# Kernel tuning notes

Hardware: AMD Instinct MI355X
Metric: run time of the kernel (lower is better)

## Reference

```python
import jax, jax.numpy as jnp
from jax import lax
import numpy as np

N, E = 10000, 120000
IN_DIM = 128
HID = 32        # hidden_dim
HEADS = 8
OUT = 32        # out_dim
HD = HID * HEADS  # 256
EPS = 1e-5


def _bn(x, g, b):
    # BatchNorm1d (training-mode batch stats, deterministic reference)
    mu = x.mean(0)
    var = x.var(0)
    return g * (x - mu) * lax.rsqrt(var + EPS) + b


def _seg_softmax(logits, seg, n):
    # softmax over edges grouped by destination node, per head
    m = jax.ops.segment_max(logits, seg, num_segments=n)
    ex = jnp.exp(logits - m[seg])
    s = jax.ops.segment_sum(ex, seg, num_segments=n)
    return ex / (s[seg] + 1e-16)


def _gat_layer(h, src, dst, fc_w, a_l, a_r, bn_g, bn_b, heads, out, residual):
    n = h.shape[0]
    h_in = h
    feat = (h @ fc_w).reshape(n, heads, out)      # [N,H,D]
    el = (feat * a_l).sum(-1)                     # [N,H]
    er = (feat * a_r).sum(-1)
    logits = jax.nn.leaky_relu(el[src] + er[dst], 0.2)  # [E,H]
    alpha = _seg_softmax(logits, dst, n)
    rst = jax.ops.segment_sum(alpha[..., None] * feat[src], dst, num_segments=n)
    rst = rst.reshape(n, heads * out)
    rst = _bn(rst, bn_g, bn_b)
    rst = jax.nn.elu(rst)
    if residual:
        rst = h_in + rst
    return rst


def setup_inputs():
    key = jax.random.key(0)
    ks = jax.random.split(key, 20)
    s = 0.02
    d = {}
    d["h"] = jax.random.normal(ks[0], (N, IN_DIM), jnp.float32)
    d["e"] = jax.random.normal(ks[1], (E, IN_DIM), jnp.float32)
    d["src"] = jax.random.randint(ks[2], (E,), 0, N, jnp.int32)
    d["dst"] = jax.random.randint(ks[3], (E,), 0, N, jnp.int32)
    d["W_emb"] = jax.random.normal(ks[4], (IN_DIM, HD)) * s
    d["b_emb"] = jnp.zeros((HD,))
    d["W_p1"] = jax.random.normal(ks[5], (IN_DIM, HID * HID)) * s
    d["b_p1"] = jnp.zeros((HID * HID,))
    d["W_p2"] = jax.random.normal(ks[6], (IN_DIM, HID)) * s
    d["b_p2"] = jnp.zeros((HID,))
    d["W_conv"] = jax.random.normal(ks[7], (1, 2, 3)) * s  # Conv1d(2->1,k=3)
    d["b_conv"] = jnp.zeros((1,))
    d["W_ep2"] = jax.random.normal(ks[8], (IN_DIM, HD)) * s
    d["b_ep2"] = jnp.zeros((HD,))
    d["W_ep3"] = jax.random.normal(ks[9], (HID, HD)) * s
    d["b_ep3"] = jnp.zeros((HD,))
    d["bn_g"] = jnp.ones((HD,))
    d["bn_b"] = jnp.zeros((HD,))
    d["fc1"] = jax.random.normal(ks[10], (HD, HD)) * s
    d["al1"] = jax.random.normal(ks[11], (HEADS, HID)) * s
    d["ar1"] = jax.random.normal(ks[12], (HEADS, HID)) * s
    d["g1"] = jnp.ones((HD,))
    d["b1"] = jnp.zeros((HD,))
    d["fc2"] = jax.random.normal(ks[13], (HD, OUT)) * s
    d["al2"] = jax.random.normal(ks[14], (1, OUT)) * s
    d["ar2"] = jax.random.normal(ks[15], (1, OUT)) * s
    d["g2"] = jnp.ones((OUT,))
    d["b2"] = jnp.zeros((OUT,))
    return d


def reference(h, e, src, dst, W_emb, b_emb, W_p1, b_p1, W_p2, b_p2,
              W_conv, b_conv, W_ep2, b_ep2, W_ep3, b_ep3, bn_g, bn_b,
              fc1, al1, ar1, g1, b1, fc2, al2, ar2, g2, b2):
    # local edge feature: Conv1d over stacked (src,dst) node feats
    edge = jnp.stack([h[src], h[dst]], axis=1)  # [E,2,IN_DIM]
    conv = lax.conv_general_dilated(edge, W_conv, (1,), [(1, 1)],
                                    dimension_numbers=("NCH", "OIH", "NCH"))
    lr_local = conv[:, 0, :] + b_conv[0]         # [E,IN_DIM]
    lr_e_local = lr_local @ W_ep2 + b_ep2        # [E,HD]
    # low-rank global affinity: mm[i,j,k] = sum_d p1[i,k,d]*p2[j,d],
    # gathered only at edges (same math as the dense NxNxHID tensor)
    p1 = (h @ W_p1 + b_p1).reshape(-1, HID, HID)  # [N,HID,HID]
    p2 = h @ W_p2 + b_p2                          # [N,HID]
    lr_glob = jnp.einsum("ekd,ed->ek", p1[src], p2[dst])  # [E,HID]
    lr_e_global = lr_glob @ W_ep3 + b_ep3        # [E,HD]
    e_feat = jax.nn.relu(_bn(lr_e_local + lr_e_global, bn_g, bn_b))
    del e_feat  # default 'dgl' GATLayer ignores e; kept for faithfulness of math
    hh = h @ W_emb + b_emb                       # embedding_h
    hh = _gat_layer(hh, src, dst, fc1, al1, ar1, g1, b1, HEADS, HID, True)
    hh = _gat_layer(hh, src, dst, fc2, al2, ar2, g2, b2, 1, OUT, False)
    return hh
```

## Files before the change

kernel.cpp:

```cpp
#include <hip/hip_runtime.h>
#include <hip/hip_bf16.h>
#include <math.h>


#define HDIM 256
#define NHEADS 8
#define ODIM 32

typedef unsigned short u16;
typedef __attribute__((ext_vector_type(8))) short short8;
typedef __attribute__((ext_vector_type(4))) float f32x4;

__device__ __forceinline__ float bf2f(u16 u) { return __uint_as_float(((unsigned)u) << 16); }
__device__ __forceinline__ u16 f2bf(float f) {
    unsigned x = __float_as_uint(f);
    return (u16)((x + 0x7FFFu + ((x >> 16) & 1u)) >> 16);
}

__global__ __launch_bounds__(256) void prep_kernel(const float* __restrict__ in_h, const float* __restrict__ W_emb,
                                                   const float* __restrict__ fc1, const float* __restrict__ fc2,
                                                   const int* __restrict__ dstv, int* __restrict__ deg,
                                                   u16* __restrict__ Ah, u16* __restrict__ Bemb,
                                                   u16* __restrict__ Bfc1, u16* __restrict__ Bfc2,
                                                   int n4, int E, int N) {
    int job = blockIdx.y;
    int idx = blockIdx.x * 256 + threadIdx.x;
    if (job == 0) {
        if (idx >= n4) return;
        float4 v = ((const float4*)in_h)[idx];
        ushort4 o = {f2bf(v.x), f2bf(v.y), f2bf(v.z), f2bf(v.w)};
        ((ushort4*)Ah)[idx] = o;
        return;
    }
    if (job == 4) {
        if (idx < E) {
            unsigned d = (unsigned)dstv[idx];
            if (d < (unsigned)N) atomicAdd(&deg[d], 1);
        }
        return;
    }
    const float* B;
    u16* O;
    int K, NC;
    if (job == 1) { B = W_emb; O = Bemb; K = 128; NC = 256; }
    else if (job == 2) { B = fc1; O = Bfc1; K = 256; NC = 256; }
    else { B = fc2; O = Bfc2; K = 256; NC = 32; }
    int KB = K / 32;
    int TOT = (NC / 16) * KB * 64;
    if (idx >= TOT) return;
    int lane = idx & 63;
    int kb = (idx >> 6) % KB;
    int ct = (idx >> 6) / KB;
    int n = ct * 16 + (lane & 15);
    int k0 = kb * 32 + (lane >> 4) * 8;
    u16* dst = O + (size_t)idx * 8;
#pragma unroll
    for (int j = 0; j < 8; j++) dst[j] = f2bf(B[(size_t)(k0 + j) * NC + n]);
}

__global__ __launch_bounds__(256) void scan_kernel(const int* __restrict__ deg, int* __restrict__ offs,
                                                   int* __restrict__ cursor, int n) {
    __shared__ int wsum[4];
    int t = threadIdx.x;
    int chunk = (n + 255) / 256;
    int lo = t * chunk, hi = lo + chunk;
    if (hi > n) hi = n;
    if (lo > n) lo = n;
    int s = 0;
    for (int i = lo; i < hi; i++) s += deg[i];
    int v = s;
#pragma unroll
    for (int d = 1; d < 64; d <<= 1) {
        int nb = __shfl_up(v, d, 64);
        if ((t & 63) >= d) v += nb;
    }
    if ((t & 63) == 63) wsum[t >> 6] = v;
    __syncthreads();
    int woff = 0;
#pragma unroll
    for (int w = 0; w < 4; w++)
        if (w < (t >> 6)) woff += wsum[w];
    int run = woff + v - s;
    for (int i = lo; i < hi; i++) {
        offs[i] = run;
        cursor[i] = run;
        run += deg[i];
    }
    if (t == 255) offs[n] = run;
}

__global__ __launch_bounds__(256) void fused_emb_fc1(const u16* __restrict__ Ah, const u16* __restrict__ Bemb,
                                                     const float* __restrict__ bemb, const u16* __restrict__ Bfc1,
                                                     const float* __restrict__ al, const float* __restrict__ ar,
                                                     u16* __restrict__ hh, u16* __restrict__ feat1,
                                                     u16* __restrict__ el, u16* __restrict__ er,
                                                     const int* __restrict__ src, const int* __restrict__ dstv,
                                                     int* __restrict__ cursor, int* __restrict__ srcs,
                                                     int M, int NB, int E, int N) {
    if ((int)blockIdx.x >= NB) {
        int i = ((int)blockIdx.x - NB) * 256 + (int)threadIdx.x;
        if (i < E) {
            unsigned d = (unsigned)dstv[i];
            if (d < (unsigned)N) {
                int p = atomicAdd(&cursor[d], 1);
                if ((unsigned)p < (unsigned)E) srcs[p] = src[i];
            }
        }
        return;
    }
    __shared__ u16 tile[16 * 256];
    const int t = threadIdx.x;
    const int lane = t & 63, w = t >> 6;
    const int rb = (int)blockIdx.x * 16;
    const int m = lane & 15, q = lane >> 4;
    const int arow = rb + m;

    short8 a0[4];
#pragma unroll
    for (int kb = 0; kb < 4; kb++) {
        if (arow < M) a0[kb] = *(const short8*)(Ah + (size_t)arow * 128 + kb * 32 + q * 8);
        else a0[kb] = (short8){0, 0, 0, 0, 0, 0, 0, 0};
    }
    const short8* B8 = (const short8*)Bemb;
#pragma unroll
    for (int ct2 = 0; ct2 < 4; ct2++) {
        const int ct = w * 4 + ct2;
        f32x4 acc = {0.f, 0.f, 0.f, 0.f};
#pragma unroll
        for (int kb = 0; kb < 4; kb++)
            acc = __builtin_amdgcn_mfma_f32_16x16x32_bf16(a0[kb], B8[(ct * 4 + kb) * 64 + lane], acc, 0, 0, 0);
        float bv = bemb[ct * 16 + m];
#pragma unroll
        for (int r = 0; r < 4; r++) {
            int rl = q * 4 + r;
            int ro = rb + rl;
            u16 hv = 0;
            if (ro < M) {
                hv = f2bf(acc[r] + bv);
                hh[(size_t)ro * 256 + ct * 16 + m] = hv;
            }
            int byte = rl * 512 + (ct * 16 + m) * 2;
            tile[(byte ^ ((rl & 7) << 4)) >> 1] = hv;
        }
    }
    __syncthreads();

    short8 af[8];
    {
        int rl = m;
#pragma unroll
        for (int kb = 0; kb < 8; kb++) {
            int byte = rl * 512 + kb * 64 + q * 16;
            af[kb] = *(const short8*)(tile + ((byte ^ ((rl & 7) << 4)) >> 1));
        }
    }
    __syncthreads();

    const short8* Bf = (const short8*)Bfc1;
#pragma unroll
    for (int ct2 = 0; ct2 < 4; ct2++) {
        const int ct = w * 4 + ct2;
        f32x4 acc = {0.f, 0.f, 0.f, 0.f};
#pragma unroll
        for (int kb = 0; kb < 8; kb++)
            acc = __builtin_amdgcn_mfma_f32_16x16x32_bf16(af[kb], Bf[(ct * 8 + kb) * 64 + lane], acc, 0, 0, 0);
#pragma unroll
        for (int r = 0; r < 4; r++) {
            int rl = q * 4 + r;
            int ro = rb + rl;
            u16 v = 0;
            if (ro < M) {
                v = f2bf(acc[r]);
                feat1[(size_t)ro * 256 + ct * 16 + m] = v;
            }
            tile[rl * 256 + ct * 16 + m] = v;
        }
    }
    __syncthreads();

    if (t < 128) {
        int nl = t >> 3, h2 = t & 7;
        int node = rb + nl;
        if (node < M) {
            float a_ = 0.f, b_ = 0.f;
#pragma unroll
            for (int d = 0; d < 32; d++) {
                float fv = bf2f(tile[nl * 256 + h2 * 32 + d]);
                a_ += fv * al[h2 * 32 + d];
                b_ += fv * ar[h2 * 32 + d];
            }
            el[node * 8 + h2] = f2bf(a_);
            er[node * 8 + h2] = f2bf(b_);
        }
    }
}

__device__ __forceinline__ float edgew(float l) {
    l = (l > 0.f) ? l : 0.2f * l;
    l = fminf(fmaxf(l, -30.f), 30.f);
    return __expf(l);
}

__global__ __launch_bounds__(256) void agg1_fused(const u16* __restrict__ feat, const u16* __restrict__ el,
                                                  const u16* __restrict__ er, const int* __restrict__ offs,
                                                  const int* __restrict__ srcs, u16* __restrict__ rst, int N, int E) {
    const int node = blockIdx.x * 4 + (threadIdx.x >> 6);
    const int lane = threadIdx.x & 63;
    if (node >= N) return;
    const int h = lane >> 3;
    int beg = offs[node], end = offs[node + 1];
    if (beg < 0) beg = 0;
    if (end > E) end = E;
    float ern = bf2f(er[node * 8 + h]);
    float ax = 0.f, ay = 0.f, az = 0.f, aw = 0.f, sw = 0.f;
    int j = beg;
    int end4 = beg + ((end - beg) & ~3);
    for (; j < end4; j += 4) {
        int s0 = srcs[j], s1 = srcs[j + 1], s2 = srcs[j + 2], s3 = srcs[j + 3];
        unsigned c0 = (unsigned)s0 < (unsigned)N, c1 = (unsigned)s1 < (unsigned)N;
        unsigned c2 = (unsigned)s2 < (unsigned)N, c3 = (unsigned)s3 < (unsigned)N;
        s0 = c0 ? s0 : 0; s1 = c1 ? s1 : 0; s2 = c2 ? s2 : 0; s3 = c3 ? s3 : 0;
        u16 e0 = el[s0 * 8 + h], e1 = el[s1 * 8 + h], e2 = el[s2 * 8 + h], e3 = el[s3 * 8 + h];
        ushort4 f0 = *(const ushort4*)(feat + (size_t)s0 * 256 + lane * 4);
        ushort4 f1 = *(const ushort4*)(feat + (size_t)s1 * 256 + lane * 4);
        ushort4 f2 = *(const ushort4*)(feat + (size_t)s2 * 256 + lane * 4);
        ushort4 f3 = *(const ushort4*)(feat + (size_t)s3 * 256 + lane * 4);
        float w0 = c0 ? edgew(bf2f(e0) + ern) : 0.f;
        float w1 = c1 ? edgew(bf2f(e1) + ern) : 0.f;
        float w2 = c2 ? edgew(bf2f(e2) + ern) : 0.f;
        float w3 = c3 ? edgew(bf2f(e3) + ern) : 0.f;
        sw += w0 + w1 + w2 + w3;
        ax += w0 * bf2f(f0.x) + w1 * bf2f(f1.x) + w2 * bf2f(f2.x) + w3 * bf2f(f3.x);
        ay += w0 * bf2f(f0.y) + w1 * bf2f(f1.y) + w2 * bf2f(f2.y) + w3 * bf2f(f3.y);
        az += w0 * bf2f(f0.z) + w1 * bf2f(f1.z) + w2 * bf2f(f2.z) + w3 * bf2f(f3.z);
        aw += w0 * bf2f(f0.w) + w1 * bf2f(f1.w) + w2 * bf2f(f2.w) + w3 * bf2f(f3.w);
    }
    for (; j < end; j++) {
        int s = srcs[j];
        if ((unsigned)s >= (unsigned)N) continue;
        float wv = edgew(bf2f(el[s * 8 + h]) + ern);
        ushort4 f4 = *(const ushort4*)(feat + (size_t)s * 256 + lane * 4);
        sw += wv;
        ax += wv * bf2f(f4.x);
        ay += wv * bf2f(f4.y);
        az += wv * bf2f(f4.z);
        aw += wv * bf2f(f4.w);
    }
    float inv = 1.f / (sw + 1e-16f);
    ushort4 o;
    o.x = f2bf(ax * inv); o.y = f2bf(ay * inv); o.z = f2bf(az * inv); o.w = f2bf(aw * inv);
    *(ushort4*)(rst + (size_t)node * 256 + lane * 4) = o;
}

__global__ __launch_bounds__(256) void bn_stats256(const u16* __restrict__ X, float* __restrict__ stats,
                                                   int rows, int RPB) {
    int t = threadIdx.x;
    int rbeg = blockIdx.x * RPB;
    int rend = rbeg + RPB;
    if (rend > rows) rend = rows;
    float s = 0.f, s2 = 0.f;
    for (int r = rbeg; r < rend; r++) {
        float x = bf2f(X[(long)r * 256 + t]);
        s += x;
        s2 += x * x;
    }
    atomicAdd(&stats[t], s);
    atomicAdd(&stats[256 + t], s2);
}

__global__ __launch_bounds__(256) void bn_stats32(const float* __restrict__ X, float* __restrict__ stats,
                                                  int rows, int RPB) {
    __shared__ float ss[256], ss2[256];
    int t = threadIdx.x, c = t & 31, rs = t >> 5;
    int rbeg = blockIdx.x * RPB;
    int rend = rbeg + RPB;
    if (rend > rows) rend = rows;
    float s = 0.f, s2 = 0.f;
    for (int r = rbeg + rs; r < rend; r += 8) {
        float x = X[(long)r * 32 + c];
        s += x;
        s2 += x * x;
    }
    ss[t] = s;
    ss2[t] = s2;
    __syncthreads();
    if (t < 32) {
        for (int j = 32; j < 256; j += 32) { s += ss[t + j]; s2 += ss2[t + j]; }
        atomicAdd(&stats[c], s);
        atomicAdd(&stats[32 + c], s2);
    }
}

__global__ __launch_bounds__(256) void gemm_fc2_fused(const u16* __restrict__ rst, const u16* __restrict__ hh,
                                                      const float* __restrict__ stats, const float* __restrict__ g,
                                                      const float* __restrict__ b, const u16* __restrict__ Bsw,
                                                      const float* __restrict__ al2, const float* __restrict__ ar2,
                                                      float* __restrict__ feat2, float* __restrict__ el2,
                                                      float* __restrict__ er2, int M, float invN) {
    __shared__ float sc[256], sh[256];
    __shared__ float red[2][256];
    __shared__ float tile[16][32];
    const int t = threadIdx.x;
    {
        float mu = stats[t] * invN;
        float var = fmaxf(stats[256 + t] * invN - mu * mu, 0.f);
        float s = g[t] * rsqrtf(var + 1e-5f);
        sc[t] = s;
        sh[t] = b[t] - mu * s;
    }
    __syncthreads();
    const int lane = t & 63, w = t >> 6;
    const int ct = w & 1, kh = w >> 1;
    const int rb = (int)blockIdx.x * 16;
    const int m = lane & 15, q = lane >> 4;
    const int row = rb + m;
    short8 a[4];
#pragma unroll
    for (int j = 0; j < 4; j++) {
        if (row < M) {
            int k0 = (kh * 4 + j) * 32 + q * 8;
            ushort4 r01 = *(const ushort4*)(rst + (size_t)row * 256 + k0);
            ushort4 r23 = *(const ushort4*)(rst + (size_t)row * 256 + k0 + 4);
            ushort4 h01 = *(const ushort4*)(hh + (size_t)row * 256 + k0);
            ushort4 h23 = *(const ushort4*)(hh + (size_t)row * 256 + k0 + 4);
            u16 rv[8] = {r01.x, r01.y, r01.z, r01.w, r23.x, r23.y, r23.z, r23.w};
            u16 hv[8] = {h01.x, h01.y, h01.z, h01.w, h23.x, h23.y, h23.z, h23.w};
            short8 av;
#pragma unroll
            for (int jj = 0; jj < 8; jj++) {
                int c = k0 + jj;
                float y = sc[c] * bf2f(rv[jj]) + sh[c];
                y = (y > 0.f) ? y : expm1f(y);
                av[jj] = (short)f2bf(bf2f(hv[jj]) + y);
            }
            a[j] = av;
        } else a[j] = (short8){0, 0, 0, 0, 0, 0, 0, 0};
    }
    const short8* B8 = (const short8*)Bsw;
    f32x4 acc = {0.f, 0.f, 0.f, 0.f};
#pragma unroll
    for (int j = 0; j < 4; j++)
        acc = __builtin_amdgcn_mfma_f32_16x16x32_bf16(a[j], B8[(ct * 8 + kh * 4 + j) * 64 + lane], acc, 0, 0, 0);
    if (kh == 1) *(f32x4*)&red[ct][lane * 4] = acc;
    __syncthreads();
    if (kh == 0) {
        f32x4 p = *(const f32x4*)&red[ct][lane * 4];
#pragma unroll
        for (int r = 0; r < 4; r++) {
            int rl = q * 4 + r;
            int ro = rb + rl;
            float v = 0.f;
            if (ro < M) {
                v = acc[r] + p[r];
                feat2[(size_t)ro * 32 + ct * 16 + m] = v;
            }
            tile[rl][ct * 16 + m] = v;
        }
    }
    __syncthreads();
    if (t < 16) {
        int node = rb + t;
        if (node < M) {
            float a_ = 0.f, b_ = 0.f;
#pragma unroll
            for (int d = 0; d < 32; d++) {
                float fv = tile[t][d];
                a_ += fv * al2[d];
                b_ += fv * ar2[d];
            }
            el2[node] = a_;
            er2[node] = b_;
        }
    }
}

__global__ __launch_bounds__(256) void agg2_fused(const float* __restrict__ feat, const float* __restrict__ el,
                                                  const float* __restrict__ er, const int* __restrict__ offs,
                                                  const int* __restrict__ srcs, float* __restrict__ rst,
                                                  int N, int E) {
    const int t = threadIdx.x;
    const int node = blockIdx.x * 8 + (t >> 5);
    const int d = t & 31;
    if (node >= N) return;
    int beg = offs[node], end = offs[node + 1];
    if (beg < 0) beg = 0;
    if (end > E) end = E;
    float ern = er[node];
    float acc = 0.f, sw = 0.f;
#pragma unroll 2
    for (int j = beg; j < end; j++) {
        int s = srcs[j];
        if ((unsigned)s >= (unsigned)N) continue;
        float wv = edgew(el[s] + ern);
        sw += wv;
        acc += wv * feat[(size_t)s * 32 + d];
    }
    rst[(size_t)node * 32 + d] = acc / (sw + 1e-16f);
}

__global__ __launch_bounds__(256) void bn_apply2(const float* __restrict__ rst, const float* __restrict__ stats,
                                                 const float* __restrict__ g, const float* __restrict__ b,
                                                 float* __restrict__ out, int total, float invN) {
    int idx = blockIdx.x * 256 + threadIdx.x;
    if (idx >= total) return;
    int c = idx & 31;
    float mu = stats[c] * invN;
    float var = fmaxf(stats[32 + c] * invN - mu * mu, 0.f);
    float y = g[c] * (rst[idx] - mu) * rsqrtf(var + 1e-5f) + b[c];
    y = (y > 0.f) ? y : expm1f(y);
    out[idx] = y;
}

extern "C" void kernel_launch(void* const* d_in, const int* in_sizes, int n_in, void* d_out, int out_size, void* d_ws,
                              size_t ws_size, hipStream_t stream) {
    const int N = out_size / ODIM;
    const int E = in_sizes[2];

    const int* src = (const int*)d_in[2];
    const int* dst = (const int*)d_in[3];
    const float* in_h = (const float*)d_in[0];
    const float* W_emb = (const float*)d_in[4];  const float* b_emb = (const float*)d_in[5];
    const float* fc1 = (const float*)d_in[18];   const float* al1 = (const float*)d_in[19];
    const float* ar1 = (const float*)d_in[20];
    const float* g1 = (const float*)d_in[21];    const float* b1 = (const float*)d_in[22];
    const float* fc2 = (const float*)d_in[23];   const float* al2 = (const float*)d_in[24];
    const float* ar2 = (const float*)d_in[25];
    const float* g2 = (const float*)d_in[26];    const float* b2 = (const float*)d_in[27];
    float* out = (float*)d_out;

    char* base = (char*)d_ws;
    size_t off = 0;
    auto alloc = [&](size_t bytes) { void* p = base + off; off += (bytes + 63) & ~63ull; return p; };
    char* zb   = (char*)alloc((size_t)N * 4 + 512 * 4 + 64 * 4);
    int* deg   = (int*)zb;
    float* stats  = (float*)(zb + (size_t)N * 4);
    float* stats2 = stats + 512;
    int* offs  = (int*)alloc((size_t)(N + 1) * 4);
    int* cursor = (int*)alloc((size_t)N * 4);
    int* srcs  = (int*)alloc((size_t)E * 4);
    u16* Ah    = (u16*)alloc((size_t)N * 128 * 2);
    u16* Bemb  = (u16*)alloc((size_t)128 * 256 * 2);
    u16* Bfc1  = (u16*)alloc((size_t)256 * 256 * 2);
    u16* Bfc2  = (u16*)alloc((size_t)256 * 32 * 2);
    u16* hh    = (u16*)alloc((size_t)N * HDIM * 2);
    u16* feat1 = (u16*)alloc((size_t)N * HDIM * 2);
    u16* el1   = (u16*)alloc((size_t)N * 8 * 2);
    u16* er1   = (u16*)alloc((size_t)N * 8 * 2);
    u16* rst   = (u16*)alloc((size_t)N * HDIM * 2);
    float* feat2 = (float*)alloc((size_t)N * 32 * 4);
    float* el2 = (float*)alloc((size_t)N * 4);
    float* er2 = (float*)alloc((size_t)N * 4);
    float* rst2 = (float*)alloc((size_t)N * 32 * 4);

    const int NB16 = (N + 15) / 16;
    const int NBF = (E + 255) / 256;

    hipMemsetAsync(zb, 0, (size_t)N * 4 + 512 * 4 + 64 * 4, stream);
    prep_kernel<<<dim3((N * 128 / 4 + 255) / 256, 5), 256, 0, stream>>>(in_h, W_emb, fc1, fc2, dst, deg,
                                                                        Ah, Bemb, Bfc1, Bfc2, N * 128 / 4, E, N);
    scan_kernel<<<1, 256, 0, stream>>>(deg, offs, cursor, N);
    fused_emb_fc1<<<NB16 + NBF, 256, 0, stream>>>(Ah, Bemb, b_emb, Bfc1, al1, ar1, hh, feat1, el1, er1,
                                                  src, dst, cursor, srcs, N, NB16, E, N);
    agg1_fused<<<(N + 3) / 4, 256, 0, stream>>>(feat1, el1, er1, offs, srcs, rst, N, E);
    bn_stats256<<<(N + 39) / 40, 256, 0, stream>>>(rst, stats, N, 40);
    gemm_fc2_fused<<<NB16, 256, 0, stream>>>(rst, hh, stats, g1, b1, Bfc2, al2, ar2, feat2, el2, er2, N, 1.f / N);
    agg2_fused<<<(N + 7) / 8, 256, 0, stream>>>(feat2, el2, er2, offs, srcs, rst2, N, E);
    bn_stats32<<<(N + 63) / 64, 256, 0, stream>>>(rst2, stats2, N, 64);
    bn_apply2<<<(N * ODIM + 255) / 256, 256, 0, stream>>>(rst2, stats2, g2, b2, out, N * ODIM, 1.f / N);
}
```

Before: 252.0 us.

## Fuse all pipeline stages into one persistent kernel with grid barriers

Replaces the sequence of nine kernel launches with a single persistent megakernel. It is sized from occupancy queries and separates stages with a software grid-wide barrier built on an atomic counter and generation flag. Each former kernel becomes a grid-stride loop inside that one kernel. The goal is to remove launch overhead and inter-kernel gaps. The cost is a spin-wait barrier with a timeout guard, lower occupancy from the shared register budget, and a deadlock risk if the blocks are not all co-resident.

Measured after the change: 449.9 us. 1.79x slower.

```diff
diff --git a/kernel.cpp b/kernel.cpp
--- a/kernel.cpp
+++ b/kernel.cpp
@@ -4,7 +4,6 @@
 
 
 #define HDIM 256
-#define NHEADS 8
 #define ODIM 32
 
 typedef unsigned short u16;
@@ -16,399 +15,439 @@
     unsigned x = __float_as_uint(f);
     return (u16)((x + 0x7FFFu + ((x >> 16) & 1u)) >> 16);
 }
-
-__global__ __launch_bounds__(256) void prep_kernel(const float* __restrict__ in_h, const float* __restrict__ W_emb,
-                                                   const float* __restrict__ fc1, const float* __restrict__ fc2,
-                                                   const int* __restrict__ dstv, int* __restrict__ deg,
-                                                   u16* __restrict__ Ah, u16* __restrict__ Bemb,
-                                                   u16* __restrict__ Bfc1, u16* __restrict__ Bfc2,
-                                                   int n4, int E, int N) {
-    int job = blockIdx.y;
-    int idx = blockIdx.x * 256 + threadIdx.x;
-    if (job == 0) {
-        if (idx >= n4) return;
-        float4 v = ((const float4*)in_h)[idx];
-        ushort4 o = {f2bf(v.x), f2bf(v.y), f2bf(v.z), f2bf(v.w)};
-        ((ushort4*)Ah)[idx] = o;
-        return;
-    }
-    if (job == 4) {
-        if (idx < E) {
-            unsigned d = (unsigned)dstv[idx];
-            if (d < (unsigned)N) atomicAdd(&deg[d], 1);
-        }
-        return;
-    }
-    const float* B;
-    u16* O;
-    int K, NC;
-    if (job == 1) { B = W_emb; O = Bemb; K = 128; NC = 256; }
-    else if (job == 2) { B = fc1; O = Bfc1; K = 256; NC = 256; }
-    else { B = fc2; O = Bfc2; K = 256; NC = 32; }
-    int KB = K / 32;
-    int TOT = (NC / 16) * KB * 64;
-    if (idx >= TOT) return;
-    int lane = idx & 63;
-    int kb = (idx >> 6) % KB;
-    int ct = (idx >> 6) / KB;
-    int n = ct * 16 + (lane & 15);
-    int k0 = kb * 32 + (lane >> 4) * 8;
-    u16* dst = O + (size_t)idx * 8;
-#pragma unroll
-    for (int j = 0; j < 8; j++) dst[j] = f2bf(B[(size_t)(k0 + j) * NC + n]);
-}
-
-__global__ __launch_bounds__(256) void scan_kernel(const int* __restrict__ deg, int* __restrict__ offs,
-                                                   int* __restrict__ cursor, int n) {
-    __shared__ int wsum[4];
-    int t = threadIdx.x;
-    int chunk = (n + 255) / 256;
-    int lo = t * chunk, hi = lo + chunk;
-    if (hi > n) hi = n;
-    if (lo > n) lo = n;
-    int s = 0;
-    for (int i = lo; i < hi; i++) s += deg[i];
-    int v = s;
-#pragma unroll
-    for (int d = 1; d < 64; d <<= 1) {
-        int nb = __shfl_up(v, d, 64);
-        if ((t & 63) >= d) v += nb;
-    }
-    if ((t & 63) == 63) wsum[t >> 6] = v;
-    __syncthreads();
-    int woff = 0;
-#pragma unroll
-    for (int w = 0; w < 4; w++)
-        if (w < (t >> 6)) woff += wsum[w];
-    int run = woff + v - s;
-    for (int i = lo; i < hi; i++) {
-        offs[i] = run;
-        cursor[i] = run;
-        run += deg[i];
-    }
-    if (t == 255) offs[n] = run;
-}
-
-__global__ __launch_bounds__(256) void fused_emb_fc1(const u16* __restrict__ Ah, const u16* __restrict__ Bemb,
-                                                     const float* __restrict__ bemb, const u16* __restrict__ Bfc1,
-                                                     const float* __restrict__ al, const float* __restrict__ ar,
-                                                     u16* __restrict__ hh, u16* __restrict__ feat1,
-                                                     u16* __restrict__ el, u16* __restrict__ er,
-                                                     const int* __restrict__ src, const int* __restrict__ dstv,
-                                                     int* __restrict__ cursor, int* __restrict__ srcs,
-                                                     int M, int NB, int E, int N) {
-    if ((int)blockIdx.x >= NB) {
-        int i = ((int)blockIdx.x - NB) * 256 + (int)threadIdx.x;
-        if (i < E) {
-            unsigned d = (unsigned)dstv[i];
-            if (d < (unsigned)N) {
-                int p = atomicAdd(&cursor[d], 1);
-                if ((unsigned)p < (unsigned)E) srcs[p] = src[i];
-            }
-        }
-        return;
-    }
-    __shared__ u16 tile[16 * 256];
-    const int t = threadIdx.x;
-    const int lane = t & 63, w = t >> 6;
-    const int rb = (int)blockIdx.x * 16;
-    const int m = lane & 15, q = lane >> 4;
-    const int arow = rb + m;
-
-    short8 a0[4];
-#pragma unroll
-    for (int kb = 0; kb < 4; kb++) {
-        if (arow < M) a0[kb] = *(const short8*)(Ah + (size_t)arow * 128 + kb * 32 + q * 8);
-        else a0[kb] = (short8){0, 0, 0, 0, 0, 0, 0, 0};
-    }
-    const short8* B8 = (const short8*)Bemb;
-#pragma unroll
-    for (int ct2 = 0; ct2 < 4; ct2++) {
-        const int ct = w * 4 + ct2;
-        f32x4 acc = {0.f, 0.f, 0.f, 0.f};
-#pragma unroll
-        for (int kb = 0; kb < 4; kb++)
-            acc = __builtin_amdgcn_mfma_f32_16x16x32_bf16(a0[kb], B8[(ct * 4 + kb) * 64 + lane], acc, 0, 0, 0);
-        float bv = bemb[ct * 16 + m];
-#pragma unroll
-        for (int r = 0; r < 4; r++) {
-            int rl = q * 4 + r;
-            int ro = rb + rl;
-            u16 hv = 0;
-            if (ro < M) {
-                hv = f2bf(acc[r] + bv);
-                hh[(size_t)ro * 256 + ct * 16 + m] = hv;
-            }
-            int byte = rl * 512 + (ct * 16 + m) * 2;
-            tile[(byte ^ ((rl & 7) << 4)) >> 1] = hv;
-        }
-    }
-    __syncthreads();
-
-    short8 af[8];
-    {
-        int rl = m;
-#pragma unroll
-        for (int kb = 0; kb < 8; kb++) {
-            int byte = rl * 512 + kb * 64 + q * 16;
-            af[kb] = *(const short8*)(tile + ((byte ^ ((rl & 7) << 4)) >> 1));
-        }
-    }
-    __syncthreads();
-
-    const short8* Bf = (const short8*)Bfc1;
-#pragma unroll
-    for (int ct2 = 0; ct2 < 4; ct2++) {
-        const int ct = w * 4 + ct2;
-        f32x4 acc = {0.f, 0.f, 0.f, 0.f};
-#pragma unroll
-        for (int kb = 0; kb < 8; kb++)
-            acc = __builtin_amdgcn_mfma_f32_16x16x32_bf16(af[kb], Bf[(ct * 8 + kb) * 64 + lane], acc, 0, 0, 0);
-#pragma unroll
-        for (int r = 0; r < 4; r++) {
-            int rl = q * 4 + r;
-            int ro = rb + rl;
-            u16 v = 0;
-            if (ro < M) {
-                v = f2bf(acc[r]);
-                feat1[(size_t)ro * 256 + ct * 16 + m] = v;
-            }
-            tile[rl * 256 + ct * 16 + m] = v;
-        }
-    }
-    __syncthreads();
-
-    if (t < 128) {
-        int nl = t >> 3, h2 = t & 7;
-        int node = rb + nl;
-        if (node < M) {
-            float a_ = 0.f, b_ = 0.f;
-#pragma unroll
-            for (int d = 0; d < 32; d++) {
-                float fv = bf2f(tile[nl * 256 + h2 * 32 + d]);
-                a_ += fv * al[h2 * 32 + d];
-                b_ += fv * ar[h2 * 32 + d];
-            }
-            el[node * 8 + h2] = f2bf(a_);
-            er[node * 8 + h2] = f2bf(b_);
-        }
-    }
-}
-
 __device__ __forceinline__ float edgew(float l) {
     l = (l > 0.f) ? l : 0.2f * l;
     l = fminf(fmaxf(l, -30.f), 30.f);
     return __expf(l);
 }
 
-__global__ __launch_bounds__(256) void agg1_fused(const u16* __restrict__ feat, const u16* __restrict__ el,
-                                                  const u16* __restrict__ er, const int* __restrict__ offs,
-                                                  const int* __restrict__ srcs, u16* __restrict__ rst, int N, int E) {
-    const int node = blockIdx.x * 4 + (threadIdx.x >> 6);
-    const int lane = threadIdx.x & 63;
-    if (node >= N) return;
-    const int h = lane >> 3;
-    int beg = offs[node], end = offs[node + 1];
-    if (beg < 0) beg = 0;
-    if (end > E) end = E;
-    float ern = bf2f(er[node * 8 + h]);
-    float ax = 0.f, ay = 0.f, az = 0.f, aw = 0.f, sw = 0.f;
-    int j = beg;
-    int end4 = beg + ((end - beg) & ~3);
-    for (; j < end4; j += 4) {
-        int s0 = srcs[j], s1 = srcs[j + 1], s2 = srcs[j + 2], s3 = srcs[j + 3];
-        unsigned c0 = (unsigned)s0 < (unsigned)N, c1 = (unsigned)s1 < (unsigned)N;
-        unsigned c2 = (unsigned)s2 < (unsigned)N, c3 = (unsigned)s3 < (unsigned)N;
-        s0 = c0 ? s0 : 0; s1 = c1 ? s1 : 0; s2 = c2 ? s2 : 0; s3 = c3 ? s3 : 0;
-        u16 e0 = el[s0 * 8 + h], e1 = el[s1 * 8 + h], e2 = el[s2 * 8 + h], e3 = el[s3 * 8 + h];
-        ushort4 f0 = *(const ushort4*)(feat + (size_t)s0 * 256 + lane * 4);
-        ushort4 f1 = *(const ushort4*)(feat + (size_t)s1 * 256 + lane * 4);
-        ushort4 f2 = *(const ushort4*)(feat + (size_t)s2 * 256 + lane * 4);
-        ushort4 f3 = *(const ushort4*)(feat + (size_t)s3 * 256 + lane * 4);
-        float w0 = c0 ? edgew(bf2f(e0) + ern) : 0.f;
-        float w1 = c1 ? edgew(bf2f(e1) + ern) : 0.f;
-        float w2 = c2 ? edgew(bf2f(e2) + ern) : 0.f;
-        float w3 = c3 ? edgew(bf2f(e3) + ern) : 0.f;
-        sw += w0 + w1 + w2 + w3;
-        ax += w0 * bf2f(f0.x) + w1 * bf2f(f1.x) + w2 * bf2f(f2.x) + w3 * bf2f(f3.x);
-        ay += w0 * bf2f(f0.y) + w1 * bf2f(f1.y) + w2 * bf2f(f2.y) + w3 * bf2f(f3.y);
-        az += w0 * bf2f(f0.z) + w1 * bf2f(f1.z) + w2 * bf2f(f2.z) + w3 * bf2f(f3.z);
-        aw += w0 * bf2f(f0.w) + w1 * bf2f(f1.w) + w2 * bf2f(f2.w) + w3 * bf2f(f3.w);
-    }
-    for (; j < end; j++) {
-        int s = srcs[j];
-        if ((unsigned)s >= (unsigned)N) continue;
-        float wv = edgew(bf2f(el[s * 8 + h]) + ern);
-        ushort4 f4 = *(const ushort4*)(feat + (size_t)s * 256 + lane * 4);
-        sw += wv;
-        ax += wv * bf2f(f4.x);
-        ay += wv * bf2f(f4.y);
-        az += wv * bf2f(f4.z);
-        aw += wv * bf2f(f4.w);
-    }
-    float inv = 1.f / (sw + 1e-16f);
-    ushort4 o;
-    o.x = f2bf(ax * inv); o.y = f2bf(ay * inv); o.z = f2bf(az * inv); o.w = f2bf(aw * inv);
-    *(ushort4*)(rst + (size_t)node * 256 + lane * 4) = o;
+__device__ __forceinline__ void gbar(int* cnt, int* gen, int nb, int it) {
+    __syncthreads();
+    if (threadIdx.x == 0) {
+        __threadfence();
+        int prev = atomicAdd(cnt, 1);
+        if (prev == nb * (it + 1) - 1) {
+            atomicExch(gen, it + 1);
+        } else {
+            long guard = 0;
+            while (atomicAdd(gen, 0) < it + 1) {
+                __builtin_amdgcn_s_sleep(2);
+                if (++guard > (1L << 24)) break;
+            }
+        }
+        __threadfence();
+    }
+    __syncthreads();
 }
 
-__global__ __launch_bounds__(256) void bn_stats256(const u16* __restrict__ X, float* __restrict__ stats,
-                                                   int rows, int RPB) {
-    int t = threadIdx.x;
-    int rbeg = blockIdx.x * RPB;
-    int rend = rbeg + RPB;
-    if (rend > rows) rend = rows;
-    float s = 0.f, s2 = 0.f;
-    for (int r = rbeg; r < rend; r++) {
-        float x = bf2f(X[(long)r * 256 + t]);
-        s += x;
-        s2 += x * x;
-    }
-    atomicAdd(&stats[t], s);
-    atomicAdd(&stats[256 + t], s2);
-}
-
-__global__ __launch_bounds__(256) void bn_stats32(const float* __restrict__ X, float* __restrict__ stats,
-                                                  int rows, int RPB) {
-    __shared__ float ss[256], ss2[256];
-    int t = threadIdx.x, c = t & 31, rs = t >> 5;
-    int rbeg = blockIdx.x * RPB;
-    int rend = rbeg + RPB;
-    if (rend > rows) rend = rows;
-    float s = 0.f, s2 = 0.f;
-    for (int r = rbeg + rs; r < rend; r += 8) {
-        float x = X[(long)r * 32 + c];
-        s += x;
-        s2 += x * x;
-    }
-    ss[t] = s;
-    ss2[t] = s2;
-    __syncthreads();
-    if (t < 32) {
-        for (int j = 32; j < 256; j += 32) { s += ss[t + j]; s2 += ss2[t + j]; }
-        atomicAdd(&stats[c], s);
-        atomicAdd(&stats[32 + c], s2);
-    }
-}
-
-__global__ __launch_bounds__(256) void gemm_fc2_fused(const u16* __restrict__ rst, const u16* __restrict__ hh,
-                                                      const float* __restrict__ stats, const float* __restrict__ g,
-                                                      const float* __restrict__ b, const u16* __restrict__ Bsw,
-                                                      const float* __restrict__ al2, const float* __restrict__ ar2,
-                                                      float* __restrict__ feat2, float* __restrict__ el2,
-                                                      float* __restrict__ er2, int M, float invN) {
-    __shared__ float sc[256], sh[256];
-    __shared__ float red[2][256];
-    __shared__ float tile[16][32];
+struct MegaP {
+    const float *in_h, *W_emb, *fc1w, *fc2w;
+    const int *src, *dst;
+    const float *bemb, *al1, *ar1, *g1, *b1, *al2, *ar2, *g2, *b2;
+    int* deg;
+    float* stats;
+    float* stats2;
+    int *cnt, *gen;
+    int *offs, *cursor, *srcs;
+    u16 *Ah, *Bemb, *Bfc1, *Bfc2;
+    u16 *hh, *feat1, *el1, *er1, *rst;
+    float *feat2, *el2, *er2, *rst2, *out;
+    int N, E, n4, NB16, NBF;
+};
+
+__global__ __launch_bounds__(256, 4) void mega(MegaP p) {
+    __shared__ alignas(16) unsigned char smem[8192];
     const int t = threadIdx.x;
+    const int bid = (int)blockIdx.x;
+    const int GRID = (int)gridDim.x;
+    const int gtid = bid * 256 + t;
+    const int GT = GRID * 256;
+    int bi = 0;
+
+    for (int i = gtid; i < p.n4; i += GT) {
+        float4 v = ((const float4*)p.in_h)[i];
+        ushort4 o = {f2bf(v.x), f2bf(v.y), f2bf(v.z), f2bf(v.w)};
+        ((ushort4*)p.Ah)[i] = o;
+    }
+    gbar(p.cnt, p.gen, GRID, bi++);
+
+    for (int i = gtid; i < p.E; i += GT) {
+        unsigned d = (unsigned)p.dst[i];
+        if (d < (unsigned)p.N) atomicAdd(&p.deg[d], 1);
+    }
+    gbar(p.cnt, p.gen, GRID, bi++);
+
+    if (bid == 0) {
+        int* wsum = (int*)smem;
+        const int n = p.N;
+        int chunk = (n + 255) / 256;
+        int lo = t * chunk, hi = lo + chunk;
+        if (hi > n) hi = n;
+        if (lo > n) lo = n;
+        int s = 0;
+        for (int i = lo; i < hi; i++) s += p.deg[i];
+        int v = s;
+#pragma unroll
+        for (int d = 1; d < 64; d <<= 1) {
+            int nb = __shfl_up(v, d, 64);
+            if ((t & 63) >= d) v += nb;
+        }
+        if ((t & 63) == 63) wsum[t >> 6] = v;
+        __syncthreads();
+        int woff = 0;
+#pragma unroll
+        for (int w = 0; w < 4; w++)
+            if (w < (t >> 6)) woff += wsum[w];
+        int run = woff + v - s;
+        for (int i = lo; i < hi; i++) {
+            p.offs[i] = run;
+            p.cursor[i] = run;
+            run += p.deg[i];
+        }
+        if (t == 255) p.offs[n] = run;
+    } else {
+        for (int u = bid - 1; u < 52; u += GRID - 1) {
+            const float* B; u16* O; int K, NC, ub;
+            if (u < 16) { B = p.W_emb; O = p.Bemb; K = 128; NC = 256; ub = u; }
+            else if (u < 48) { B = p.fc1w; O = p.Bfc1; K = 256; NC = 256; ub = u - 16; }
+            else { B = p.fc2w; O = p.Bfc2; K = 256; NC = 32; ub = u - 48; }
+            int idx = ub * 256 + t;
+            int KB = K / 32;
+            int TOT = (NC / 16) * KB * 64;
+            if (idx < TOT) {
+                int lane = idx & 63;
+                int kb = (idx >> 6) % KB;
+                int ct = (idx >> 6) / KB;
+                int nn = ct * 16 + (lane & 15);
+                int k0 = kb * 32 + (lane >> 4) * 8;
+                u16* dstp = O + (size_t)idx * 8;
+#pragma unroll
+                for (int j = 0; j < 8; j++) dstp[j] = f2bf(B[(size_t)(k0 + j) * NC + nn]);
+            }
+        }
+    }
+    gbar(p.cnt, p.gen, GRID, bi++);
+
+    for (int u = bid; u < p.NB16 + p.NBF; u += GRID) {
+        if (u >= p.NB16) {
+            int i = (u - p.NB16) * 256 + t;
+            if (i < p.E) {
+                unsigned d = (unsigned)p.dst[i];
+                if (d < (unsigned)p.N) {
+                    int pp = atomicAdd(&p.cursor[d], 1);
+                    if ((unsigned)pp < (unsigned)p.E) p.srcs[pp] = p.src[i];
+                }
+            }
+            continue;
+        }
+        u16* tile = (u16*)smem;
+        const int lane = t & 63, w = t >> 6;
+        const int rb = u * 16;
+        const int m = lane & 15, q = lane >> 4;
+        const int arow = rb + m;
+        const int M = p.N;
+        short8 a0[4];
+#pragma unroll
+        for (int kb = 0; kb < 4; kb++) {
+            if (arow < M) a0[kb] = *(const short8*)(p.Ah + (size_t)arow * 128 + kb * 32 + q * 8);
+            else a0[kb] = (short8){0, 0, 0, 0, 0, 0, 0, 0};
+        }
+        const short8* B8 = (const short8*)p.Bemb;
+#pragma unroll
+        for (int ct2 = 0; ct2 < 4; ct2++) {
+            const int ct = w * 4 + ct2;
+            f32x4 acc = {0.f, 0.f, 0.f, 0.f};
+#pragma unroll
+            for (int kb = 0; kb < 4; kb++)
+                acc = __builtin_amdgcn_mfma_f32_16x16x32_bf16(a0[kb], B8[(ct * 4 + kb) * 64 + lane], acc, 0, 0, 0);
+            float bv = p.bemb[ct * 16 + m];
+#pragma unroll
+            for (int r = 0; r < 4; r++) {
+                int rl = q * 4 + r;
+                int ro = rb + rl;
+                u16 hv = 0;
+                if (ro < M) {
+                    hv = f2bf(acc[r] + bv);
+                    p.hh[(size_t)ro * 256 + ct * 16 + m] = hv;
+                }
+                int byte = rl * 512 + (ct * 16 + m) * 2;
+                tile[(byte ^ ((rl & 7) << 4)) >> 1] = hv;
+            }
+        }
+        __syncthreads();
+        short8 af[8];
+        {
+            int rl = m;
+#pragma unroll
+            for (int kb = 0; kb < 8; kb++) {
+                int byte = rl * 512 + kb * 64 + q * 16;
+                af[kb] = *(const short8*)(tile + ((byte ^ ((rl & 7) << 4)) >> 1));
+            }
+        }
+        __syncthreads();
+        const short8* Bf = (const short8*)p.Bfc1;
+#pragma unroll
+        for (int ct2 = 0; ct2 < 4; ct2++) {
+            const int ct = w * 4 + ct2;
+            f32x4 acc = {0.f, 0.f, 0.f, 0.f};
+#pragma unroll
+            for (int kb = 0; kb < 8; kb++)
+                acc = __builtin_amdgcn_mfma_f32_16x16x32_bf16(af[kb], Bf[(ct * 8 + kb) * 64 + lane], acc, 0, 0, 0);
+#pragma unroll
+            for (int r = 0; r < 4; r++) {
+                int rl = q * 4 + r;
+                int ro = rb + rl;
+                u16 v = 0;
+                if (ro < M) {
+                    v = f2bf(acc[r]);
+                    p.feat1[(size_t)ro * 256 + ct * 16 + m] = v;
+                }
+                tile[rl * 256 + ct * 16 + m] = v;
+            }
+        }
+        __syncthreads();
+        if (t < 128) {
+            int nl = t >> 3, h2 = t & 7;
+            int node = rb + nl;
+            if (node < M) {
+                float a_ = 0.f, b_ = 0.f;
+#pragma unroll
+                for (int d = 0; d < 32; d++) {
+                    float fv = bf2f(tile[nl * 256 + h2 * 32 + d]);
+                    a_ += fv * p.al1[h2 * 32 + d];
+                    b_ += fv * p.ar1[h2 * 32 + d];
+                }
+                p.el1[node * 8 + h2] = f2bf(a_);
+                p.er1[node * 8 + h2] = f2bf(b_);
+            }
+        }
+        __syncthreads();
+    }
+    gbar(p.cnt, p.gen, GRID, bi++);
+
     {
-        float mu = stats[t] * invN;
-        float var = fmaxf(stats[256 + t] * invN - mu * mu, 0.f);
-        float s = g[t] * rsqrtf(var + 1e-5f);
-        sc[t] = s;
-        sh[t] = b[t] - mu * s;
-    }
-    __syncthreads();
-    const int lane = t & 63, w = t >> 6;
-    const int ct = w & 1, kh = w >> 1;
-    const int rb = (int)blockIdx.x * 16;
-    const int m = lane & 15, q = lane >> 4;
-    const int row = rb + m;
-    short8 a[4];
-#pragma unroll
-    for (int j = 0; j < 4; j++) {
-        if (row < M) {
-            int k0 = (kh * 4 + j) * 32 + q * 8;
-            ushort4 r01 = *(const ushort4*)(rst + (size_t)row * 256 + k0);
-            ushort4 r23 = *(const ushort4*)(rst + (size_t)row * 256 + k0 + 4);
-            ushort4 h01 = *(const ushort4*)(hh + (size_t)row * 256 + k0);
-            ushort4 h23 = *(const ushort4*)(hh + (size_t)row * 256 + k0 + 4);
-            u16 rv[8] = {r01.x, r01.y, r01.z, r01.w, r23.x, r23.y, r23.z, r23.w};
-            u16 hv[8] = {h01.x, h01.y, h01.z, h01.w, h23.x, h23.y, h23.z, h23.w};
-            short8 av;
-#pragma unroll
-            for (int jj = 0; jj < 8; jj++) {
-                int c = k0 + jj;
-                float y = sc[c] * bf2f(rv[jj]) + sh[c];
-                y = (y > 0.f) ? y : expm1f(y);
-                av[jj] = (short)f2bf(bf2f(hv[jj]) + y);
-            }
-            a[j] = av;
-        } else a[j] = (short8){0, 0, 0, 0, 0, 0, 0, 0};
-    }
-    const short8* B8 = (const short8*)Bsw;
-    f32x4 acc = {0.f, 0.f, 0.f, 0.f};
-#pragma unroll
-    for (int j = 0; j < 4; j++)
-        acc = __builtin_amdgcn_mfma_f32_16x16x32_bf16(a[j], B8[(ct * 8 + kh * 4 + j) * 64 + lane], acc, 0, 0, 0);
-    if (kh == 1) *(f32x4*)&red[ct][lane * 4] = acc;
-    __syncthreads();
-    if (kh == 0) {
-        f32x4 p = *(const f32x4*)&red[ct][lane * 4];
-#pragma unroll
-        for (int r = 0; r < 4; r++) {
-            int rl = q * 4 + r;
-            int ro = rb + rl;
-            float v = 0.f;
-            if (ro < M) {
-                v = acc[r] + p[r];
-                feat2[(size_t)ro * 32 + ct * 16 + m] = v;
-            }
-            tile[rl][ct * 16 + m] = v;
-        }
-    }
-    __syncthreads();
-    if (t < 16) {
-        int node = rb + t;
-        if (node < M) {
-            float a_ = 0.f, b_ = 0.f;
-#pragma unroll
-            for (int d = 0; d < 32; d++) {
-                float fv = tile[t][d];
-                a_ += fv * al2[d];
-                b_ += fv * ar2[d];
-            }
-            el2[node] = a_;
-            er2[node] = b_;
-        }
-    }
-}
-
-__global__ __launch_bounds__(256) void agg2_fused(const float* __restrict__ feat, const float* __restrict__ el,
-                                                  const float* __restrict__ er, const int* __restrict__ offs,
-                                                  const int* __restrict__ srcs, float* __restrict__ rst,
-                                                  int N, int E) {
-    const int t = threadIdx.x;
-    const int node = blockIdx.x * 8 + (t >> 5);
-    const int d = t & 31;
-    if (node >= N) return;
-    int beg = offs[node], end = offs[node + 1];
-    if (beg < 0) beg = 0;
-    if (end > E) end = E;
-    float ern = er[node];
-    float acc = 0.f, sw = 0.f;
+        const int NU = (p.N + 3) >> 2;
+        for (int u = bid; u < NU; u += GRID) {
+            const int node = u * 4 + (t >> 6);
+            const int lane = t & 63;
+            if (node < p.N) {
+                const int h = lane >> 3;
+                int beg = p.offs[node], end = p.offs[node + 1];
+                if (beg < 0) beg = 0;
+                if (end > p.E) end = p.E;
+                float ern = bf2f(p.er1[node * 8 + h]);
+                float ax = 0.f, ay = 0.f, az = 0.f, aw = 0.f, sw = 0.f;
+                int j = beg;
+                int end4 = beg + ((end - beg) & ~3);
+                for (; j < end4; j += 4) {
+                    int s0 = p.srcs[j], s1 = p.srcs[j + 1], s2 = p.srcs[j + 2], s3 = p.srcs[j + 3];
+                    unsigned c0 = (unsigned)s0 < (unsigned)p.N, c1 = (unsigned)s1 < (unsigned)p.N;
+                    unsigned c2 = (unsigned)s2 < (unsigned)p.N, c3 = (unsigned)s3 < (unsigned)p.N;
+                    s0 = c0 ? s0 : 0; s1 = c1 ? s1 : 0; s2 = c2 ? s2 : 0; s3 = c3 ? s3 : 0;
+                    u16 e0 = p.el1[s0 * 8 + h], e1 = p.el1[s1 * 8 + h];
+                    u16 e2 = p.el1[s2 * 8 + h], e3 = p.el1[s3 * 8 + h];
+                    ushort4 f0 = *(const ushort4*)(p.feat1 + (size_t)s0 * 256 + lane * 4);
+                    ushort4 f1 = *(const ushort4*)(p.feat1 + (size_t)s1 * 256 + lane * 4);
+                    ushort4 f2 = *(const ushort4*)(p.feat1 + (size_t)s2 * 256 + lane * 4);
+                    ushort4 f3 = *(const ushort4*)(p.feat1 + (size_t)s3 * 256 + lane * 4);
+                    float w0 = c0 ? edgew(bf2f(e0) + ern) : 0.f;
+                    float w1 = c1 ? edgew(bf2f(e1) + ern) : 0.f;
+                    float w2 = c2 ? edgew(bf2f(e2) + ern) : 0.f;
+                    float w3 = c3 ? edgew(bf2f(e3) + ern) : 0.f;
+                    sw += w0 + w1 + w2 + w3;
+                    ax += w0 * bf2f(f0.x) + w1 * bf2f(f1.x) + w2 * bf2f(f2.x) + w3 * bf2f(f3.x);
+                    ay += w0 * bf2f(f0.y) + w1 * bf2f(f1.y) + w2 * bf2f(f2.y) + w3 * bf2f(f3.y);
+                    az += w0 * bf2f(f0.z) + w1 * bf2f(f1.z) + w2 * bf2f(f2.z) + w3 * bf2f(f3.z);
+                    aw += w0 * bf2f(f0.w) + w1 * bf2f(f1.w) + w2 * bf2f(f2.w) + w3 * bf2f(f3.w);
+                }
+                for (; j < end; j++) {
+                    int s = p.srcs[j];
+                    if ((unsigned)s >= (unsigned)p.N) continue;
+                    float wv = edgew(bf2f(p.el1[s * 8 + h]) + ern);
+                    ushort4 f4 = *(const ushort4*)(p.feat1 + (size_t)s * 256 + lane * 4);
+                    sw += wv;
+                    ax += wv * bf2f(f4.x);
+                    ay += wv * bf2f(f4.y);
+                    az += wv * bf2f(f4.z);
+                    aw += wv * bf2f(f4.w);
+                }
+                float inv = 1.f / (sw + 1e-16f);
+                ushort4 o;
+                o.x = f2bf(ax * inv); o.y = f2bf(ay * inv);
+                o.z = f2bf(az * inv); o.w = f2bf(aw * inv);
+                *(ushort4*)(p.rst + (size_t)node * 256 + lane * 4) = o;
+            }
+        }
+    }
+    gbar(p.cnt, p.gen, GRID, bi++);
+
+    {
+        const int NU = (p.N + 39) / 40;
+        for (int u = bid; u < NU; u += GRID) {
+            int rbeg = u * 40;
+            int rend = rbeg + 40;
+            if (rend > p.N) rend = p.N;
+            float s = 0.f, s2 = 0.f;
+            for (int r = rbeg; r < rend; r++) {
+                float x = bf2f(p.rst[(size_t)r * 256 + t]);
+                s += x;
+                s2 += x * x;
+            }
+            atomicAdd(&p.stats[t], s);
+            atomicAdd(&p.stats[256 + t], s2);
+        }
+    }
+    gbar(p.cnt, p.gen, GRID, bi++);
+
+    {
+        const float invN = 1.f / p.N;
+        float* sc = (float*)smem;
+        float* sh = sc + 256;
+        float* red = sh + 256;
+        float* tl = red + 512;
+        const int M = p.N;
+        for (int u = bid; u < p.NB16; u += GRID) {
+            {
+                float mu = p.stats[t] * invN;
+                float var = fmaxf(p.stats[256 + t] * invN - mu * mu, 0.f);
+                float s = p.g1[t] * rsqrtf(var + 1e-5f);
+                sc[t] = s;
+                sh[t] = p.b1[t] - mu * s;
+            }
+            __syncthreads();
+            const int lane = t & 63, w = t >> 6;
+            const int ct = w & 1, kh = w >> 1;
+            const int rb = u * 16;
+            const int m = lane & 15, q = lane >> 4;
+            const int row = rb + m;
+            short8 a[4];
+#pragma unroll
+            for (int j = 0; j < 4; j++) {
+                if (row < M) {
+                    int k0 = (kh * 4 + j) * 32 + q * 8;
+                    ushort4 r01 = *(const ushort4*)(p.rst + (size_t)row * 256 + k0);
+                    ushort4 r23 = *(const ushort4*)(p.rst + (size_t)row * 256 + k0 + 4);
+                    ushort4 h01 = *(const ushort4*)(p.hh + (size_t)row * 256 + k0);
+                    ushort4 h23 = *(const ushort4*)(p.hh + (size_t)row * 256 + k0 + 4);
+                    u16 rv[8] = {r01.x, r01.y, r01.z, r01.w, r23.x, r23.y, r23.z, r23.w};
+                    u16 hv[8] = {h01.x, h01.y, h01.z, h01.w, h23.x, h23.y, h23.z, h23.w};
+                    short8 av;
+#pragma unroll
+                    for (int jj = 0; jj < 8; jj++) {
+                        int c = k0 + jj;
+                        float y = sc[c] * bf2f(rv[jj]) + sh[c];
+                        y = (y > 0.f) ? y : expm1f(y);
+                        av[jj] = (short)f2bf(bf2f(hv[jj]) + y);
+                    }
+                    a[j] = av;
+                } else a[j] = (short8){0, 0, 0, 0, 0, 0, 0, 0};
+            }
+            const short8* B8 = (const short8*)p.Bfc2;
+            f32x4 acc = {0.f, 0.f, 0.f, 0.f};
+#pragma unroll
+            for (int j = 0; j < 4; j++)
+                acc = __builtin_amdgcn_mfma_f32_16x16x32_bf16(a[j], B8[(ct * 8 + kh * 4 + j) * 64 + lane], acc, 0, 0, 0);
+            if (kh == 1) *(f32x4*)&red[ct * 256 + lane * 4] = acc;
+            __syncthreads();
+            if (kh == 0) {
+                f32x4 pp = *(const f32x4*)&red[ct * 256 + lane * 4];
+#pragma unroll
+                for (int r = 0; r < 4; r++) {
+                    int rl = q * 4 + r;
+                    int ro = rb + rl;
+                    float v = 0.f;
+                    if (ro < M) {
+                        v = acc[r] + pp[r];
+                        p.feat2[(size_t)ro * 32 + ct * 16 + m] = v;
+                    }
+                    tl[rl * 32 + ct * 16 + m] = v;
+                }
+            }
+            __syncthreads();
+            if (t < 16) {
+                int node = rb + t;
+                if (node < M) {
+                    float a_ = 0.f, b_ = 0.f;
+#pragma unroll
+                    for (int d = 0; d < 32; d++) {
+                        float fv = tl[t * 32 + d];
+                        a_ += fv * p.al2[d];
+                        b_ += fv * p.ar2[d];
+                    }
+                    p.el2[node] = a_;
+                    p.er2[node] = b_;
+                }
+            }
+            __syncthreads();
+        }
+    }
+    gbar(p.cnt, p.gen, GRID, bi++);
+
+    {
+        const int NU = (p.N + 7) >> 3;
+        for (int u = bid; u < NU; u += GRID) {
+            const int node = u * 8 + (t >> 5);
+            const int d = t & 31;
+            if (node < p.N) {
+                int beg = p.offs[node], end = p.offs[node + 1];
+                if (beg < 0) beg = 0;
+                if (end > p.E) end = p.E;
+                float ern = p.er2[node];
+                float acc = 0.f, sw = 0.f;
 #pragma unroll 2
-    for (int j = beg; j < end; j++) {
-        int s = srcs[j];
-        if ((unsigned)s >= (unsigned)N) continue;
-        float wv = edgew(el[s] + ern);
-        sw += wv;
-        acc += wv * feat[(size_t)s * 32 + d];
-    }
-    rst[(size_t)node * 32 + d] = acc / (sw + 1e-16f);
-}
-
-__global__ __launch_bounds__(256) void bn_apply2(const float* __restrict__ rst, const float* __restrict__ stats,
-                                                 const float* __restrict__ g, const float* __restrict__ b,
-                                                 float* __restrict__ out, int total, float invN) {
-    int idx = blockIdx.x * 256 + threadIdx.x;
-    if (idx >= total) return;
-    int c = idx & 31;
-    float mu = stats[c] * invN;
-    float var = fmaxf(stats[32 + c] * invN - mu * mu, 0.f);
-    float y = g[c] * (rst[idx] - mu) * rsqrtf(var + 1e-5f) + b[c];
-    y = (y > 0.f) ? y : expm1f(y);
-    out[idx] = y;
+                for (int j = beg; j < end; j++) {
+                    int s = p.srcs[j];
+                    if ((unsigned)s >= (unsigned)p.N) continue;
+                    float wv = edgew(p.el2[s] + ern);
+                    sw += wv;
+                    acc += wv * p.feat2[(size_t)s * 32 + d];
+                }
+                p.rst2[(size_t)node * 32 + d] = acc / (sw + 1e-16f);
+            }
+        }
+    }
+    gbar(p.cnt, p.gen, GRID, bi++);
+
+    {
+        float* ss = (float*)smem;
+        float* ss2 = ss + 256;
+        const int NU = (p.N + 63) >> 6;
+        for (int u = bid; u < NU; u += GRID) {
+            int c = t & 31, rs = t >> 5;
+            int rbeg = u * 64;
+            int rend = rbeg + 64;
+            if (rend > p.N) rend = p.N;
+            float s = 0.f, s2 = 0.f;
+            for (int r = rbeg + rs; r < rend; r += 8) {
+                float x = p.rst2[(size_t)r * 32 + c];
+                s += x;
+                s2 += x * x;
+            }
+            ss[t] = s;
+            ss2[t] = s2;
+            __syncthreads();
+            if (t < 32) {
+                for (int j = 32; j < 256; j += 32) { s += ss[t + j]; s2 += ss2[t + j]; }
+                atomicAdd(&p.stats2[c], s);
+                atomicAdd(&p.stats2[32 + c], s2);
+            }
+            __syncthreads();
+        }
+    }
+    gbar(p.cnt, p.gen, GRID, bi++);
+
+    {
+        const float invN = 1.f / p.N;
+        const int total = p.N * 32;
+        for (int i = gtid; i < total; i += GT) {
+            int c = i & 31;
+            float mu = p.stats2[c] * invN;
+            float var = fmaxf(p.stats2[32 + c] * invN - mu * mu, 0.f);
+            float y = p.g2[c] * (p.rst2[i] - mu) * rsqrtf(var + 1e-5f) + p.b2[c];
+            y = (y > 0.f) ? y : expm1f(y);
+            p.out[i] = y;
+        }
+    }
 }
 
 extern "C" void kernel_launch(void* const* d_in, const int* in_sizes, int n_in, void* d_out, int out_size, void* d_ws,
@@ -416,55 +455,62 @@
     const int N = out_size / ODIM;
     const int E = in_sizes[2];
 
-    const int* src = (const int*)d_in[2];
-    const int* dst = (const int*)d_in[3];
-    const float* in_h = (const float*)d_in[0];
-    const float* W_emb = (const float*)d_in[4];  const float* b_emb = (const float*)d_in[5];
-    const float* fc1 = (const float*)d_in[18];   const float* al1 = (const float*)d_in[19];
-    const float* ar1 = (const float*)d_in[20];
-    const float* g1 = (const float*)d_in[21];    const float* b1 = (const float*)d_in[22];
-    const float* fc2 = (const float*)d_in[23];   const float* al2 = (const float*)d_in[24];
-    const float* ar2 = (const float*)d_in[25];
-    const float* g2 = (const float*)d_in[26];    const float* b2 = (const float*)d_in[27];
-    float* out = (float*)d_out;
+    MegaP P;
+    P.in_h = (const float*)d_in[0];
+    P.src = (const int*)d_in[2];
+    P.dst = (const int*)d_in[3];
+    P.W_emb = (const float*)d_in[4];  P.bemb = (const float*)d_in[5];
+    P.fc1w = (const float*)d_in[18];  P.al1 = (const float*)d_in[19];
+    P.ar1 = (const float*)d_in[20];
+    P.g1 = (const float*)d_in[21];    P.b1 = (const float*)d_in[22];
+    P.fc2w = (const float*)d_in[23];  P.al2 = (const float*)d_in[24];
+    P.ar2 = (const float*)d_in[25];
+    P.g2 = (const float*)d_in[26];    P.b2 = (const float*)d_in[27];
+    P.out = (float*)d_out;
 
     char* base = (char*)d_ws;
     size_t off = 0;
     auto alloc = [&](size_t bytes) { void* p = base + off; off += (bytes + 63) & ~63ull; return p; };
-    char* zb   = (char*)alloc((size_t)N * 4 + 512 * 4 + 64 * 4);
-    int* deg   = (int*)zb;
-    float* stats  = (float*)(zb + (size_t)N * 4);
-    float* stats2 = stats + 512;
-    int* offs  = (int*)alloc((size_t)(N + 1) * 4);
-    int* cursor = (int*)alloc((size_t)N * 4);
-    int* srcs  = (int*)alloc((size_t)E * 4);
-    u16* Ah    = (u16*)alloc((size_t)N * 128 * 2);
-    u16* Bemb  = (u16*)alloc((size_t)128 * 256 * 2);
-    u16* Bfc1  = (u16*)alloc((size_t)256 * 256 * 2);
-    u16* Bfc2  = (u16*)alloc((size_t)256 * 32 * 2);
-    u16* hh    = (u16*)alloc((size_t)N * HDIM * 2);
-    u16* feat1 = (u16*)alloc((size_t)N * HDIM * 2);
-    u16* el1   = (u16*)alloc((size_t)N * 8 * 2);
-    u16* er1   = (u16*)alloc((size_t)N * 8 * 2);
-    u16* rst   = (u16*)alloc((size_t)N * HDIM * 2);
-    float* feat2 = (float*)alloc((size_t)N * 32 * 4);
-    float* el2 = (float*)alloc((size_t)N * 4);
-    float* er2 = (float*)alloc((size_t)N * 4);
-    float* rst2 = (float*)alloc((size_t)N * 32 * 4);
-
-    const int NB16 = (N + 15) / 16;
-    const int NBF = (E + 255) / 256;
-
-    hipMemsetAsync(zb, 0, (size_t)N * 4 + 512 * 4 + 64 * 4, stream);
-    prep_kernel<<<dim3((N * 128 / 4 + 255) / 256, 5), 256, 0, stream>>>(in_h, W_emb, fc1, fc2, dst, deg,
-                                                                        Ah, Bemb, Bfc1, Bfc2, N * 128 / 4, E, N);
-    scan_kernel<<<1, 256, 0, stream>>>(deg, offs, cursor, N);
-    fused_emb_fc1<<<NB16 + NBF, 256, 0, stream>>>(Ah, Bemb, b_emb, Bfc1, al1, ar1, hh, feat1, el1, er1,
-                                                  src, dst, cursor, srcs, N, NB16, E, N);
-    agg1_fused<<<(N + 3) / 4, 256, 0, stream>>>(feat1, el1, er1, offs, srcs, rst, N, E);
-    bn_stats256<<<(N + 39) / 40, 256, 0, stream>>>(rst, stats, N, 40);
-    gemm_fc2_fused<<<NB16, 256, 0, stream>>>(rst, hh, stats, g1, b1, Bfc2, al2, ar2, feat2, el2, er2, N, 1.f / N);
-    agg2_fused<<<(N + 7) / 8, 256, 0, stream>>>(feat2, el2, er2, offs, srcs, rst2, N, E);
-    bn_stats32<<<(N + 63) / 64, 256, 0, stream>>>(rst2, stats2, N, 64);
-    bn_apply2<<<(N * ODIM + 255) / 256, 256, 0, stream>>>(rst2, stats2, g2, b2, out, N * ODIM, 1.f / N);
+    const size_t ZBYTES = (size_t)N * 4 + 512 * 4 + 64 * 4 + 256;
+    char* zb = (char*)alloc(ZBYTES);
+    P.deg = (int*)zb;
+    P.stats = (float*)(zb + (size_t)N * 4);
+    P.stats2 = P.stats + 512;
+    P.cnt = (int*)(P.stats2 + 64);
+    P.gen = P.cnt + 16;
+    P.offs = (int*)alloc((size_t)(N + 1) * 4);
+    P.cursor = (int*)alloc((size_t)N * 4);
+    P.srcs = (int*)alloc((size_t)E * 4);
+    P.Ah = (u16*)alloc((size_t)N * 128 * 2);
+    P.Bemb = (u16*)alloc((size_t)128 * 256 * 2);
+    P.Bfc1 = (u16*)alloc((size_t)256 * 256 * 2);
+    P.Bfc2 = (u16*)alloc((size_t)256 * 32 * 2);
+    P.hh = (u16*)alloc((size_t)N * HDIM * 2);
+    P.feat1 = (u16*)alloc((size_t)N * HDIM * 2);
+    P.el1 = (u16*)alloc((size_t)N * 8 * 2);
+    P.er1 = (u16*)alloc((size_t)N * 8 * 2);
+    P.rst = (u16*)alloc((size_t)N * HDIM * 2);
+    P.feat2 = (float*)alloc((size_t)N * 32 * 4);
+    P.el2 = (float*)alloc((size_t)N * 4);
+    P.er2 = (float*)alloc((size_t)N * 4);
+    P.rst2 = (float*)alloc((size_t)N * 32 * 4);
+
+    P.N = N;
+    P.E = E;
+    P.n4 = N * 32;
+    P.NB16 = (N + 15) / 16;
+    P.NBF = (E + 255) / 256;
+
+    static int g_grid = 0;
+    if (g_grid == 0) {
+        int nb = 0;
+        hipError_t e =
+            hipOccupancyMaxActiveBlocksPerMultiprocessor(&nb, reinterpret_cast<const void*>(mega), 256, 0);
+        if (e != hipSuccess || nb < 1) nb = 1;
+        if (nb > 4) nb = 4;
+        g_grid = nb * 256;
+    }
+
+    hipMemsetAsync(zb, 0, ZBYTES, stream);
+    mega<<<dim3(g_grid), dim3(256), 0, stream>>>(P);
 }
```
